# Performance work log

Measured on AMD Instinct MI355X. Metric: run time of the kernel, lower is better.

The kernel has to match this reference:

```python
import jax, jax.numpy as jnp
import numpy as np

E = 128      # embedding_dim
H = 128      # hidden_dim
A = 4        # n_ary
DEPTH = 8    # complete 4-ary tree depth (root at level 0)
N_NODES = (A ** (DEPTH + 1) - 1) // (A - 1)  # 87381


def setup_inputs() -> dict:
    key = jax.random.key(0)
    ks = jax.random.split(key, 11)
    s = 0.05  # weight scale to keep gates in a sane range
    return {
        "embeddings": jax.random.normal(ks[0], (N_NODES, E), jnp.float32),
        "W_iou": jax.random.normal(ks[1], (3 * H, E), jnp.float32) * s,
        "b_iou": jax.random.normal(ks[2], (3 * H,), jnp.float32) * s,
        "U_iou": jax.random.normal(ks[3], (3 * H, A * H), jnp.float32) * s,
        "b_uiou": jax.random.normal(ks[4], (3 * H,), jnp.float32) * s,
        "W_f": jax.random.normal(ks[5], (H, E), jnp.float32) * s,
        "b_wf": jax.random.normal(ks[6], (H,), jnp.float32) * s,
        "U_f": jax.random.normal(ks[7], (A * H, A * H), jnp.float32) * s,
        "b_uf": jax.random.normal(ks[8], (A * H,), jnp.float32) * s,
        "h0": jax.random.uniform(ks[9], (1, A * H), jnp.float32),
        "c0": jax.random.uniform(ks[10], (1, A * H), jnp.float32),
    }


def _tree_lstm_cell(x, h, c, W_iou, b_iou, U_iou, b_uiou, W_f, b_wf, U_f, b_uf):
    # x: [n, E], h/c: [n, A*H]
    n = x.shape[0]
    iou = x @ W_iou.T + b_iou + h @ U_iou.T + b_uiou          # [n, 3H]
    i, o, u = jnp.split(iou, 3, axis=1)
    # forget gates: one per child slot, broadcast W_f(x) over arity dim
    f = jax.nn.sigmoid((h @ U_f.T + b_uf).reshape(n, A, H)
                       + (x @ W_f.T + b_wf)[:, None, :])       # [n, A, H]
    c_new = jax.nn.sigmoid(i) * jnp.tanh(u) + jnp.sum(f * c.reshape(n, A, H), axis=1)
    h_new = jax.nn.sigmoid(o) * jnp.tanh(c_new)
    return h_new, c_new


def reference(embeddings, W_iou, b_iou, U_iou, b_uiou, W_f, b_wf, U_f, b_uf, h0, c0):
    # Level-synchronized bottom-up pass over a complete 4-ary tree of depth DEPTH.
    # embeddings are ordered deepest-level-first; children of parent i at level l
    # are nodes 4i..4i+3 of level l+1.
    hs, cs = [], []
    off = 0
    n_leaf = A ** DEPTH
    h_in = jnp.tile(h0, (n_leaf, 1))  # leaves use learned initial state
    c_in = jnp.tile(c0, (n_leaf, 1))
    for l in range(DEPTH, -1, -1):
        n = A ** l
        x = embeddings[off:off + n]
        h_new, c_new = _tree_lstm_cell(x, h_in, c_in,
                                       W_iou, b_iou, U_iou, b_uiou,
                                       W_f, b_wf, U_f, b_uf)
        hs.append(h_new)
        cs.append(c_new)
        off += n
        if l > 0:
            # pack each parent's A children states into one [A*H] vector
            h_in = h_new.reshape(n // A, A * H)
            c_in = c_new.reshape(n // A, A * H)
    out_h = jnp.concatenate(hs, axis=0)[None]  # [1, N_NODES, H]
    out_c = jnp.concatenate(cs, axis=0)[None]  # [1, N_NODES, H]
    return out_h, out_c
```

## Files before the change

### kernel.cpp

```cpp
#include <hip/hip_runtime.h>
#include <hip/hip_bf16.h>

#define NNODES   87381
#define KIN      640
#define NOUTS    896
#define WC_ELEMS (NOUTS * KIN)
#define DG_STRIDE  71680
#define KT_STRIDE2 3584

typedef __attribute__((ext_vector_type(8))) unsigned short ushort8;
typedef __attribute__((ext_vector_type(4))) unsigned short ushort4v;
typedef __attribute__((ext_vector_type(8))) __bf16        bf16x8;
typedef __attribute__((ext_vector_type(4))) float         f32x4;

union Frag8 { ushort8 u; bf16x8 b; };

__device__ __forceinline__ unsigned short f2bf(float f) {
    unsigned int x = __float_as_uint(f);
    x += 0x7fffu + ((x >> 16) & 1u);
    return (unsigned short)(x >> 16);
}
__device__ __forceinline__ float sigf(float x) {
    return __builtin_amdgcn_rcpf(1.0f + __expf(-x));
}
__device__ __forceinline__ float tanh_fast(float x) { return 2.0f * sigf(2.0f * x) - 1.0f; }

__global__ __launch_bounds__(512) void build_wc(
    const float* __restrict__ W_iou, const float* __restrict__ U_iou,
    const float* __restrict__ W_f,   const float* __restrict__ U_f,
    unsigned short* __restrict__ Wc)
{
    int idx = blockIdx.x * 512 + threadIdx.x;
    if (idx >= WC_ELEMS) return;
    int dg = idx / DG_STRIDE;
    int r  = idx - dg * DG_STRIDE;
    int kt = r / KT_STRIDE2;
    int r2 = r - kt * KT_STRIDE2;
    int cf = r2 >> 9;
    int r3 = r2 & 511;
    int ln = r3 >> 3;
    int j  = r3 & 7;
    int out = cf * 128 + dg * 16 + (ln & 15);
    int k   = kt * 32 + ((ln >> 4) << 3) + j;
    float v;
    if (out < 384) {
        v = (k < 128) ? W_iou[out * 128 + k] : U_iou[(size_t)out * 512 + (k - 128)];
    } else {
        int o2 = out - 384;
        v = (k < 128) ? W_f[(o2 & 127) * 128 + k] : U_f[(size_t)o2 * 512 + (k - 128)];
    }
    Wc[idx] = f2bf(v);
}

__global__ __launch_bounds__(512) void build_consts(
    const float* __restrict__ U_iou, const float* __restrict__ U_f,
    const float* __restrict__ b_iou, const float* __restrict__ b_uiou,
    const float* __restrict__ b_wf,  const float* __restrict__ b_uf,
    const float* __restrict__ h0,
    float* __restrict__ biasc, float* __restrict__ hUc)
{
    const int o  = blockIdx.x * 8 + (threadIdx.x >> 6);
    const int ln = threadIdx.x & 63;
    if (o >= NOUTS) return;
    const float* Urow = (o < 384) ? (U_iou + (size_t)o * 512)
                                  : (U_f + (size_t)(o - 384) * 512);
    const float4 u0 = *(const float4*)(Urow + ln * 8);
    const float4 u1 = *(const float4*)(Urow + ln * 8 + 4);
    const float4 h0v = *(const float4*)(h0 + ln * 8);
    const float4 h1v = *(const float4*)(h0 + ln * 8 + 4);
    float s = u0.x*h0v.x + u0.y*h0v.y + u0.z*h0v.z + u0.w*h0v.w
            + u1.x*h1v.x + u1.y*h1v.y + u1.z*h1v.z + u1.w*h1v.w;
    #pragma unroll
    for (int w = 32; w >= 1; w >>= 1) s += __shfl_xor(s, w);
    if (ln == 0) {
        float b = (o < 384) ? (b_iou[o] + b_uiou[o])
                            : (b_wf[(o - 384) & 127] + b_uf[o - 384]);
        biasc[o] = b;
        hUc[o]   = b + s;
    }
}

__global__ __launch_bounds__(512) void tree_leaf32(
    const float* __restrict__ emb, const unsigned short* __restrict__ Wc,
    const float* __restrict__ hUc, const float* __restrict__ c0,
    float* __restrict__ outh, float* __restrict__ outc,
    unsigned short* __restrict__ hb)
{
    __shared__ __align__(16) char lds[8192];
    const int tid   = threadIdx.x;
    const int node0 = blockIdx.x * 32;

    {
        const int srow = tid >> 4;
        const int sc4  = (tid & 15) << 2;
        const float* src = emb + (size_t)(node0 + srow) * 128;
        const float4 v0 = *(const float4*)(src + sc4);
        const float4 v1 = *(const float4*)(src + 64 + sc4);
        const unsigned wby = (unsigned)((srow * 128 + sc4 * 2) ^ ((srow & 7) << 4));
        ushort4v w0, w1;
        w0[0] = f2bf(v0.x); w0[1] = f2bf(v0.y); w0[2] = f2bf(v0.z); w0[3] = f2bf(v0.w);
        w1[0] = f2bf(v1.x); w1[1] = f2bf(v1.y); w1[2] = f2bf(v1.z); w1[3] = f2bf(v1.w);
        *(ushort4v*)(lds + wby)        = w0;
        *(ushort4v*)(lds + 4096 + wby) = w1;
    }
    __syncthreads();

    const int wv = tid >> 6, ln = tid & 63, grp = ln >> 4, cl = ln & 15;
    const unsigned short* wbase = Wc + (size_t)wv * DG_STRIDE + (size_t)ln * 8;

    f32x4 acc[2][7] = {};
    #pragma unroll
    for (int kt = 0; kt < 4; ++kt) {
        const unsigned short* kp = wbase + kt * KT_STRIDE2;
        Frag8 bfr[7];
        #pragma unroll
        for (int cf = 0; cf < 7; ++cf)
            bfr[cf].u = *(const ushort8*)(kp + cf * 512);
        #pragma unroll
        for (int rf = 0; rf < 2; ++rf) {
            const int row = rf * 16 + cl;
            Frag8 afr;
            afr.u = *(const ushort8*)(lds + (kt >> 1) * 4096 + row * 128
                                      + (((kt & 1) * 64 + grp * 16) ^ ((row & 7) << 4)));
            #pragma unroll
            for (int cf = 0; cf < 7; ++cf)
                acc[rf][cf] = __builtin_amdgcn_mfma_f32_16x16x32_bf16(
                    afr.b, bfr[cf].b, acc[rf][cf], 0, 0, 0);
        }
    }

    const int d = wv * 16 + cl;
    const float bi = hUc[d];
    const float bo = hUc[128 + d];
    const float bu = hUc[256 + d];
    float bfa[4], cin_leaf[4];
    #pragma unroll
    for (int a = 0; a < 4; ++a) { bfa[a] = hUc[384 + a * 128 + d]; cin_leaf[a] = c0[a * 128 + d]; }

    #pragma unroll
    for (int rf = 0; rf < 2; ++rf) {
        #pragma unroll
        for (int reg = 0; reg < 4; ++reg) {
            const int m = node0 + rf * 16 + grp * 4 + reg;
            const float i_ = acc[rf][0][reg] + bi;
            const float o_ = acc[rf][1][reg] + bo;
            const float u_ = acc[rf][2][reg] + bu;
            float c_ = sigf(i_) * tanh_fast(u_);
            #pragma unroll
            for (int a = 0; a < 4; ++a)
                c_ += sigf(acc[rf][3 + a][reg] + bfa[a]) * cin_leaf[a];
            const float h_ = sigf(o_) * tanh_fast(c_);
            const size_t oidx = (size_t)m * 128 + d;
            outh[oidx] = h_;
            outc[oidx] = c_;
            hb[oidx]   = f2bf(h_);
        }
    }
}

__global__ __launch_bounds__(512) void tree_dsplit(
    const float* __restrict__ emb, const unsigned short* __restrict__ Wc,
    const float* __restrict__ biasc,
    float* __restrict__ outh, float* __restrict__ outc,
    unsigned short* __restrict__ hb,
    int n, int off, int cb)
{
    __shared__ __align__(16) char lds[43008];
    const int tid   = threadIdx.x;
    const int mt    = blockIdx.x >> 3;
    const int dg    = blockIdx.x & 7;
    const int node0 = mt * 32;

    {
        const int srow = tid >> 4;
        const int sc4  = (tid & 15) << 2;
        int r = node0 + srow; if (r >= n) r = n - 1;
        const unsigned wby = (unsigned)((srow * 128 + sc4 * 2) ^ ((srow & 7) << 4));
        const float4 v0 = *(const float4*)(emb + (size_t)(off + r) * 128 + sc4);
        const float4 v1 = *(const float4*)(emb + (size_t)(off + r) * 128 + 64 + sc4);
        ushort4v w[10];
        #pragma unroll
        for (int i = 2; i < 10; ++i)
            w[i] = *(const ushort4v*)(hb + (size_t)(cb + 4 * r + ((i - 2) >> 1)) * 128
                                         + ((i - 2) & 1) * 64 + sc4);
        w[0][0] = f2bf(v0.x); w[0][1] = f2bf(v0.y); w[0][2] = f2bf(v0.z); w[0][3] = f2bf(v0.w);
        w[1][0] = f2bf(v1.x); w[1][1] = f2bf(v1.y); w[1][2] = f2bf(v1.z); w[1][3] = f2bf(v1.w);
        #pragma unroll
        for (int i = 0; i < 10; ++i)
            *(ushort4v*)(lds + i * 4096 + wby) = w[i];
    }
    __syncthreads();

    const int wv  = tid >> 6;
    const int ln  = tid & 63;
    const int grp = ln >> 4;
    const int cl  = ln & 15;
    const int rf  = wv & 1;
    const int kq  = wv >> 1;
    const int row = rf * 16 + cl;
    const int swr = (row & 7) << 4;

    const unsigned short* wbase = Wc + (size_t)dg * DG_STRIDE + (size_t)ln * 8
                                     + (size_t)(kq * 5) * KT_STRIDE2;

    f32x4 acc[7] = {};
    #pragma unroll
    for (int t = 0; t < 5; ++t) {
        const int kt = kq * 5 + t;
        Frag8 afr;
        afr.u = *(const ushort8*)(lds + (kt >> 1) * 4096 + row * 128
                                  + (((kt & 1) * 64 + grp * 16) ^ swr));
        const unsigned short* kp = wbase + t * KT_STRIDE2;
        Frag8 bfr[7];
        #pragma unroll
        for (int cf = 0; cf < 7; ++cf)
            bfr[cf].u = *(const ushort8*)(kp + cf * 512);
        #pragma unroll
        for (int cf = 0; cf < 7; ++cf)
            acc[cf] = __builtin_amdgcn_mfma_f32_16x16x32_bf16(
                afr.b, bfr[cf].b, acc[cf], 0, 0, 0);
    }
    __syncthreads();

    float* red = (float*)lds;
    if (kq != 0) {
        const int slot = (((kq - 1) * 2 + rf) * 64 + ln) * 28;
        #pragma unroll
        for (int cf = 0; cf < 7; ++cf)
            *(f32x4*)(red + slot + cf * 4) = acc[cf];
    }
    __syncthreads();
    if (kq == 0) {
        #pragma unroll
        for (int q = 1; q < 4; ++q) {
            const int s2 = (((q - 1) * 2 + rf) * 64 + ln) * 28;
            #pragma unroll
            for (int cf = 0; cf < 7; ++cf)
                acc[cf] += *(const f32x4*)(red + s2 + cf * 4);
        }
        const int d = dg * 16 + cl;
        const float bi = biasc[d];
        const float bo = biasc[128 + d];
        const float bu = biasc[256 + d];
        float bfa[4];
        #pragma unroll
        for (int a = 0; a < 4; ++a) bfa[a] = biasc[384 + a * 128 + d];

        #pragma unroll
        for (int reg = 0; reg < 4; ++reg) {
            const int m = node0 + rf * 16 + grp * 4 + reg;
            if (m < n) {
                const float i_ = acc[0][reg] + bi;
                const float o_ = acc[1][reg] + bo;
                const float u_ = acc[2][reg] + bu;
                float c_ = sigf(i_) * tanh_fast(u_);
                #pragma unroll
                for (int a = 0; a < 4; ++a)
                    c_ += sigf(acc[3 + a][reg] + bfa[a]) * outc[(size_t)(cb + 4 * m + a) * 128 + d];
                const float h_ = sigf(o_) * tanh_fast(c_);
                const size_t oidx = (size_t)(off + m) * 128 + d;
                outh[oidx] = h_;
                outc[oidx] = c_;
                hb[oidx]   = f2bf(h_);
            }
        }
    }
}

__global__ __launch_bounds__(512) void tree_tail3(
    const float* __restrict__ emb, const unsigned short* __restrict__ Wc,
    const float* __restrict__ biasc,
    float* __restrict__ outh, float* __restrict__ outc,
    unsigned short* __restrict__ hb)
{
    __shared__ __align__(16) char lds[40960];
    const int ns[3]   = {16, 4, 1};
    const int offs[3] = {87360, 87376, 87380};
    const int cbs[3]  = {87296, 87360, 87376};

    const int tid = threadIdx.x;
    const int wv = tid >> 6, ln = tid & 63, grp = ln >> 4, cl = ln & 15;

    #pragma unroll 1
    for (int li = 0; li < 3; ++li) {
        const int n = ns[li], off = offs[li], cb = cbs[li];

        if (tid < 256) {
            const int srow = tid >> 4;
            const int sc4  = (tid & 15) << 2;
            int r = srow; if (r >= n) r = n - 1;
            const unsigned wby = (unsigned)((srow * 128 + sc4 * 2) ^ ((srow & 7) << 4));
            const float4 v0 = *(const float4*)(emb + (size_t)(off + r) * 128 + sc4);
            const float4 v1 = *(const float4*)(emb + (size_t)(off + r) * 128 + 64 + sc4);
            ushort4v w0, w1;
            w0[0] = f2bf(v0.x); w0[1] = f2bf(v0.y); w0[2] = f2bf(v0.z); w0[3] = f2bf(v0.w);
            w1[0] = f2bf(v1.x); w1[1] = f2bf(v1.y); w1[2] = f2bf(v1.z); w1[3] = f2bf(v1.w);
            *(ushort4v*)(lds + wby)        = w0;
            *(ushort4v*)(lds + 4096 + wby) = w1;
            #pragma unroll
            for (int i = 2; i < 10; ++i) {
                ushort4v w = *(const ushort4v*)(hb + (size_t)(cb + 4 * r + ((i - 2) >> 1)) * 128
                                                   + ((i - 2) & 1) * 64 + sc4);
                *(ushort4v*)(lds + i * 4096 + wby) = w;
            }
        }
        __syncthreads();

        const unsigned short* wbase = Wc + (size_t)wv * DG_STRIDE + (size_t)ln * 8;
        f32x4 acc[7] = {};
        #pragma unroll 2
        for (int kt = 0; kt < 20; ++kt) {
            Frag8 afr;
            afr.u = *(const ushort8*)(lds + (kt >> 1) * 4096 + cl * 128
                                      + (((kt & 1) * 64 + grp * 16) ^ ((cl & 7) << 4)));
            const unsigned short* kp = wbase + kt * KT_STRIDE2;
            Frag8 bfr[7];
            #pragma unroll
            for (int cf = 0; cf < 7; ++cf)
                bfr[cf].u = *(const ushort8*)(kp + cf * 512);
            #pragma unroll
            for (int cf = 0; cf < 7; ++cf)
                acc[cf] = __builtin_amdgcn_mfma_f32_16x16x32_bf16(
                    afr.b, bfr[cf].b, acc[cf], 0, 0, 0);
        }

        const int d = wv * 16 + cl;
        const float bi = biasc[d];
        const float bo = biasc[128 + d];
        const float bu = biasc[256 + d];
        float bfa[4];
        #pragma unroll
        for (int a = 0; a < 4; ++a) bfa[a] = biasc[384 + a * 128 + d];

        #pragma unroll
        for (int reg = 0; reg < 4; ++reg) {
            const int m = grp * 4 + reg;
            if (m < n) {
                const float i_ = acc[0][reg] + bi;
                const float o_ = acc[1][reg] + bo;
                const float u_ = acc[2][reg] + bu;
                float c_ = sigf(i_) * tanh_fast(u_);
                #pragma unroll
                for (int a = 0; a < 4; ++a)
                    c_ += sigf(acc[3 + a][reg] + bfa[a]) * outc[(size_t)(cb + 4 * m + a) * 128 + d];
                const float h_ = sigf(o_) * tanh_fast(c_);
                const size_t oidx = (size_t)(off + m) * 128 + d;
                outh[oidx] = h_;
                outc[oidx] = c_;
                hb[oidx]   = f2bf(h_);
            }
        }
        __threadfence();
        __syncthreads();
    }
}

extern "C" void kernel_launch(void* const* d_in, const int* in_sizes, int n_in,
                              void* d_out, int out_size, void* d_ws, size_t ws_size,
                              hipStream_t stream)
{
    const float* emb    = (const float*)d_in[0];
    const float* W_iou  = (const float*)d_in[1];
    const float* b_iou  = (const float*)d_in[2];
    const float* U_iou  = (const float*)d_in[3];
    const float* b_uiou = (const float*)d_in[4];
    const float* W_f    = (const float*)d_in[5];
    const float* b_wf   = (const float*)d_in[6];
    const float* U_f    = (const float*)d_in[7];
    const float* b_uf   = (const float*)d_in[8];
    const float* h0     = (const float*)d_in[9];
    const float* c0     = (const float*)d_in[10];

    char* ws = (char*)d_ws;
    unsigned short* Wc  = (unsigned short*)ws;
    float* biasc        = (float*)(ws + 1146880);
    float* hUc          = (float*)(ws + 1150464);
    unsigned short* hb  = (unsigned short*)(ws + 1154112);

    float* outh = (float*)d_out;
    float* outc = outh + (size_t)NNODES * 128;

    hipLaunchKernelGGL(build_wc, dim3((WC_ELEMS + 511) / 512), dim3(512), 0, stream,
                       W_iou, U_iou, W_f, U_f, Wc);
    hipLaunchKernelGGL(build_consts, dim3(NOUTS / 8), dim3(512), 0, stream,
                       U_iou, U_f, b_iou, b_uiou, b_wf, b_uf, h0, biasc, hUc);

    hipLaunchKernelGGL(tree_leaf32, dim3(2048), dim3(512), 0, stream,
                       emb, Wc, hUc, c0, outh, outc, hb);

    const int ns[5]   = {16384, 4096, 1024, 256, 64};
    const int offs[5] = {65536, 81920, 86016, 87040, 87296};
    const int cbs[5]  = {0, 65536, 81920, 86016, 87040};
    for (int li = 0; li < 5; ++li) {
        const int units = (ns[li] / 32) * 8;
        hipLaunchKernelGGL(tree_dsplit, dim3(units), dim3(512), 0, stream,
                           emb, Wc, biasc, outh, outc, hb,
                           ns[li], offs[li], cbs[li]);
    }

    hipLaunchKernelGGL(tree_tail3, dim3(1), dim3(512), 0, stream,
                       emb, Wc, biasc, outh, outc, hb);
}
```

Before: 320.8 us.

## Merge prep kernels, widen staging loads, remap blocks per XCD, double-buffer weight fragments

Fuses the weight-packing and bias/constant kernels into a single prep launch to save one launch. Staging loads of embeddings and child hidden states now use 16-byte vectors, so each thread issues fewer global and LDS operations. tree_dsplit remaps block indices so that consecutive node tiles land on the same XCD, which should improve L2 locality. It also double-buffers the weight B-fragments across k-steps to overlap global loads with MFMA, at the cost of more registers.

```diff
diff --git a/kernel.cpp b/kernel.cpp
--- a/kernel.cpp
+++ b/kernel.cpp
@@ -9,7 +9,6 @@
 #define KT_STRIDE2 3584
 
 typedef __attribute__((ext_vector_type(8))) unsigned short ushort8;
-typedef __attribute__((ext_vector_type(4))) unsigned short ushort4v;
 typedef __attribute__((ext_vector_type(8))) __bf16        bf16x8;
 typedef __attribute__((ext_vector_type(4))) float         f32x4;
 
@@ -25,58 +24,61 @@
 }
 __device__ __forceinline__ float tanh_fast(float x) { return 2.0f * sigf(2.0f * x) - 1.0f; }
 
-__global__ __launch_bounds__(512) void build_wc(
+__device__ __forceinline__ ushort8 pack8(const float4& v0, const float4& v1) {
+    ushort8 w;
+    w[0] = f2bf(v0.x); w[1] = f2bf(v0.y); w[2] = f2bf(v0.z); w[3] = f2bf(v0.w);
+    w[4] = f2bf(v1.x); w[5] = f2bf(v1.y); w[6] = f2bf(v1.z); w[7] = f2bf(v1.w);
+    return w;
+}
+
+__global__ __launch_bounds__(512) void prep(
     const float* __restrict__ W_iou, const float* __restrict__ U_iou,
     const float* __restrict__ W_f,   const float* __restrict__ U_f,
-    unsigned short* __restrict__ Wc)
-{
-    int idx = blockIdx.x * 512 + threadIdx.x;
-    if (idx >= WC_ELEMS) return;
-    int dg = idx / DG_STRIDE;
-    int r  = idx - dg * DG_STRIDE;
-    int kt = r / KT_STRIDE2;
-    int r2 = r - kt * KT_STRIDE2;
-    int cf = r2 >> 9;
-    int r3 = r2 & 511;
-    int ln = r3 >> 3;
-    int j  = r3 & 7;
-    int out = cf * 128 + dg * 16 + (ln & 15);
-    int k   = kt * 32 + ((ln >> 4) << 3) + j;
-    float v;
-    if (out < 384) {
-        v = (k < 128) ? W_iou[out * 128 + k] : U_iou[(size_t)out * 512 + (k - 128)];
-    } else {
-        int o2 = out - 384;
-        v = (k < 128) ? W_f[(o2 & 127) * 128 + k] : U_f[(size_t)o2 * 512 + (k - 128)];
-    }
-    Wc[idx] = f2bf(v);
-}
-
-__global__ __launch_bounds__(512) void build_consts(
-    const float* __restrict__ U_iou, const float* __restrict__ U_f,
     const float* __restrict__ b_iou, const float* __restrict__ b_uiou,
     const float* __restrict__ b_wf,  const float* __restrict__ b_uf,
     const float* __restrict__ h0,
-    float* __restrict__ biasc, float* __restrict__ hUc)
+    unsigned short* __restrict__ Wc, float* __restrict__ biasc, float* __restrict__ hUc)
 {
-    const int o  = blockIdx.x * 8 + (threadIdx.x >> 6);
-    const int ln = threadIdx.x & 63;
-    if (o >= NOUTS) return;
-    const float* Urow = (o < 384) ? (U_iou + (size_t)o * 512)
-                                  : (U_f + (size_t)(o - 384) * 512);
-    const float4 u0 = *(const float4*)(Urow + ln * 8);
-    const float4 u1 = *(const float4*)(Urow + ln * 8 + 4);
-    const float4 h0v = *(const float4*)(h0 + ln * 8);
-    const float4 h1v = *(const float4*)(h0 + ln * 8 + 4);
-    float s = u0.x*h0v.x + u0.y*h0v.y + u0.z*h0v.z + u0.w*h0v.w
-            + u1.x*h1v.x + u1.y*h1v.y + u1.z*h1v.z + u1.w*h1v.w;
-    #pragma unroll
-    for (int w = 32; w >= 1; w >>= 1) s += __shfl_xor(s, w);
-    if (ln == 0) {
-        float b = (o < 384) ? (b_iou[o] + b_uiou[o])
-                            : (b_wf[(o - 384) & 127] + b_uf[o - 384]);
-        biasc[o] = b;
-        hUc[o]   = b + s;
+    if (blockIdx.x < 1120) {
+        int idx = blockIdx.x * 512 + threadIdx.x;
+        int dg = idx / DG_STRIDE;
+        int r  = idx - dg * DG_STRIDE;
+        int kt = r / KT_STRIDE2;
+        int r2 = r - kt * KT_STRIDE2;
+        int cf = r2 >> 9;
+        int r3 = r2 & 511;
+        int ln = r3 >> 3;
+        int j  = r3 & 7;
+        int out = cf * 128 + dg * 16 + (ln & 15);
+        int k   = kt * 32 + ((ln >> 4) << 3) + j;
+        float v;
+        if (out < 384) {
+            v = (k < 128) ? W_iou[out * 128 + k] : U_iou[(size_t)out * 512 + (k - 128)];
+        } else {
+            int o2 = out - 384;
+            v = (k < 128) ? W_f[(o2 & 127) * 128 + k] : U_f[(size_t)o2 * 512 + (k - 128)];
+        }
+        Wc[idx] = f2bf(v);
+    } else {
+        const int o  = (blockIdx.x - 1120) * 8 + (threadIdx.x >> 6);
+        const int ln = threadIdx.x & 63;
+        if (o >= NOUTS) return;
+        const float* Urow = (o < 384) ? (U_iou + (size_t)o * 512)
+                                      : (U_f + (size_t)(o - 384) * 512);
+        const float4 u0 = *(const float4*)(Urow + ln * 8);
+        const float4 u1 = *(const float4*)(Urow + ln * 8 + 4);
+        const float4 h0v = *(const float4*)(h0 + ln * 8);
+        const float4 h1v = *(const float4*)(h0 + ln * 8 + 4);
+        float s = u0.x*h0v.x + u0.y*h0v.y + u0.z*h0v.z + u0.w*h0v.w
+                + u1.x*h1v.x + u1.y*h1v.y + u1.z*h1v.z + u1.w*h1v.w;
+        #pragma unroll
+        for (int w = 32; w >= 1; w >>= 1) s += __shfl_xor(s, w);
+        if (ln == 0) {
+            float b = (o < 384) ? (b_iou[o] + b_uiou[o])
+                                : (b_wf[(o - 384) & 127] + b_uf[o - 384]);
+            biasc[o] = b;
+            hUc[o]   = b + s;
+        }
     }
 }
 
@@ -92,16 +94,13 @@
 
     {
         const int srow = tid >> 4;
-        const int sc4  = (tid & 15) << 2;
-        const float* src = emb + (size_t)(node0 + srow) * 128;
-        const float4 v0 = *(const float4*)(src + sc4);
-        const float4 v1 = *(const float4*)(src + 64 + sc4);
-        const unsigned wby = (unsigned)((srow * 128 + sc4 * 2) ^ ((srow & 7) << 4));
-        ushort4v w0, w1;
-        w0[0] = f2bf(v0.x); w0[1] = f2bf(v0.y); w0[2] = f2bf(v0.z); w0[3] = f2bf(v0.w);
-        w1[0] = f2bf(v1.x); w1[1] = f2bf(v1.y); w1[2] = f2bf(v1.z); w1[3] = f2bf(v1.w);
-        *(ushort4v*)(lds + wby)        = w0;
-        *(ushort4v*)(lds + 4096 + wby) = w1;
+        const int q    = tid & 15;
+        const float* src = emb + (size_t)(node0 + srow) * 128 + q * 8;
+        const float4 v0 = *(const float4*)src;
+        const float4 v1 = *(const float4*)(src + 4);
+        const int stripe = q >> 3;
+        const unsigned by = (unsigned)((srow * 128 + (q & 7) * 16) ^ ((srow & 7) << 4));
+        *(ushort8*)(lds + stripe * 4096 + by) = pack8(v0, v1);
     }
     __syncthreads();
 
@@ -166,28 +165,44 @@
     int n, int off, int cb)
 {
     __shared__ __align__(16) char lds[43008];
-    const int tid   = threadIdx.x;
-    const int mt    = blockIdx.x >> 3;
-    const int dg    = blockIdx.x & 7;
+    const int tid = threadIdx.x;
+    const int nmt = n >> 5;
+
+    int mt, dg;
+    if (nmt >= 8) {
+        const int xcd = blockIdx.x & 7;
+        const int j   = blockIdx.x >> 3;
+        mt = xcd * (nmt >> 3) + (j >> 3);
+        dg = j & 7;
+    } else {
+        mt = blockIdx.x >> 3;
+        dg = blockIdx.x & 7;
+    }
     const int node0 = mt * 32;
 
     {
         const int srow = tid >> 4;
-        const int sc4  = (tid & 15) << 2;
+        const int q    = tid & 15;
         int r = node0 + srow; if (r >= n) r = n - 1;
-        const unsigned wby = (unsigned)((srow * 128 + sc4 * 2) ^ ((srow & 7) << 4));
-        const float4 v0 = *(const float4*)(emb + (size_t)(off + r) * 128 + sc4);
-        const float4 v1 = *(const float4*)(emb + (size_t)(off + r) * 128 + 64 + sc4);
-        ushort4v w[10];
-        #pragma unroll
-        for (int i = 2; i < 10; ++i)
-            w[i] = *(const ushort4v*)(hb + (size_t)(cb + 4 * r + ((i - 2) >> 1)) * 128
-                                         + ((i - 2) & 1) * 64 + sc4);
-        w[0][0] = f2bf(v0.x); w[0][1] = f2bf(v0.y); w[0][2] = f2bf(v0.z); w[0][3] = f2bf(v0.w);
-        w[1][0] = f2bf(v1.x); w[1][1] = f2bf(v1.y); w[1][2] = f2bf(v1.z); w[1][3] = f2bf(v1.w);
-        #pragma unroll
-        for (int i = 0; i < 10; ++i)
-            *(ushort4v*)(lds + i * 4096 + wby) = w[i];
+        const unsigned sx = (unsigned)((srow & 7) << 4);
+        {
+            const float* s = emb + (size_t)(off + r) * 128 + q * 8;
+            const float4 v0 = *(const float4*)s;
+            const float4 v1 = *(const float4*)(s + 4);
+            const int stripe = q >> 3;
+            const unsigned by = (unsigned)((srow * 128 + (q & 7) * 16) ^ sx);
+            *(ushort8*)(lds + stripe * 4096 + by) = pack8(v0, v1);
+        }
+        #pragma unroll
+        for (int c = 1; c < 5; ++c) {
+            const int e = c * 128 + q * 8;
+            const int child = (e - 128) >> 7;
+            const int d0    = (e - 128) & 127;
+            ushort8 w = *(const ushort8*)(hb + (size_t)(cb + 4 * r + child) * 128 + d0);
+            const int stripe = e >> 6;
+            const unsigned by = (unsigned)((srow * 128 + (e & 63) * 2) ^ sx);
+            *(ushort8*)(lds + stripe * 4096 + by) = w;
+        }
     }
     __syncthreads();
 
@@ -203,22 +218,29 @@
     const unsigned short* wbase = Wc + (size_t)dg * DG_STRIDE + (size_t)ln * 8
                                      + (size_t)(kq * 5) * KT_STRIDE2;
 
+    Frag8 bb[2][7];
+    #pragma unroll
+    for (int cf = 0; cf < 7; ++cf)
+        bb[0][cf].u = *(const ushort8*)(wbase + cf * 512);
+
     f32x4 acc[7] = {};
     #pragma unroll
     for (int t = 0; t < 5; ++t) {
+        const int cur = t & 1, nxt = cur ^ 1;
+        if (t < 4) {
+            const unsigned short* kp = wbase + (t + 1) * KT_STRIDE2;
+            #pragma unroll
+            for (int cf = 0; cf < 7; ++cf)
+                bb[nxt][cf].u = *(const ushort8*)(kp + cf * 512);
+        }
         const int kt = kq * 5 + t;
         Frag8 afr;
         afr.u = *(const ushort8*)(lds + (kt >> 1) * 4096 + row * 128
                                   + (((kt & 1) * 64 + grp * 16) ^ swr));
-        const unsigned short* kp = wbase + t * KT_STRIDE2;
-        Frag8 bfr[7];
-        #pragma unroll
-        for (int cf = 0; cf < 7; ++cf)
-            bfr[cf].u = *(const ushort8*)(kp + cf * 512);
         #pragma unroll
         for (int cf = 0; cf < 7; ++cf)
             acc[cf] = __builtin_amdgcn_mfma_f32_16x16x32_bf16(
-                afr.b, bfr[cf].b, acc[cf], 0, 0, 0);
+                afr.b, bb[cur][cf].b, acc[cf], 0, 0, 0);
     }
     __syncthreads();
 
@@ -287,21 +309,24 @@
 
         if (tid < 256) {
             const int srow = tid >> 4;
-            const int sc4  = (tid & 15) << 2;
+            const int q    = tid & 15;
             int r = srow; if (r >= n) r = n - 1;
-            const unsigned wby = (unsigned)((srow * 128 + sc4 * 2) ^ ((srow & 7) << 4));
-            const float4 v0 = *(const float4*)(emb + (size_t)(off + r) * 128 + sc4);
-            const float4 v1 = *(const float4*)(emb + (size_t)(off + r) * 128 + 64 + sc4);
-            ushort4v w0, w1;
-            w0[0] = f2bf(v0.x); w0[1] = f2bf(v0.y); w0[2] = f2bf(v0.z); w0[3] = f2bf(v0.w);
-            w1[0] = f2bf(v1.x); w1[1] = f2bf(v1.y); w1[2] = f2bf(v1.z); w1[3] = f2bf(v1.w);
-            *(ushort4v*)(lds + wby)        = w0;
-            *(ushort4v*)(lds + 4096 + wby) = w1;
-            #pragma unroll
-            for (int i = 2; i < 10; ++i) {
-                ushort4v w = *(const ushort4v*)(hb + (size_t)(cb + 4 * r + ((i - 2) >> 1)) * 128
-                                                   + ((i - 2) & 1) * 64 + sc4);
-                *(ushort4v*)(lds + i * 4096 + wby) = w;
+            const unsigned sx = (unsigned)((srow & 7) << 4);
+            {
+                const float* s = emb + (size_t)(off + r) * 128 + q * 8;
+                const float4 v0 = *(const float4*)s;
+                const float4 v1 = *(const float4*)(s + 4);
+                const unsigned by = (unsigned)((srow * 128 + (q & 7) * 16) ^ sx);
+                *(ushort8*)(lds + (q >> 3) * 4096 + by) = pack8(v0, v1);
+            }
+            #pragma unroll
+            for (int c = 1; c < 5; ++c) {
+                const int e = c * 128 + q * 8;
+                const int child = (e - 128) >> 7;
+                const int d0    = (e - 128) & 127;
+                ushort8 w = *(const ushort8*)(hb + (size_t)(cb + 4 * r + child) * 128 + d0);
+                const unsigned by = (unsigned)((srow * 128 + (e & 63) * 2) ^ sx);
+                *(ushort8*)(lds + (e >> 6) * 4096 + by) = w;
             }
         }
         __syncthreads();
@@ -380,10 +405,9 @@
     float* outh = (float*)d_out;
     float* outc = outh + (size_t)NNODES * 128;
 
-    hipLaunchKernelGGL(build_wc, dim3((WC_ELEMS + 511) / 512), dim3(512), 0, stream,
-                       W_iou, U_iou, W_f, U_f, Wc);
-    hipLaunchKernelGGL(build_consts, dim3(NOUTS / 8), dim3(512), 0, stream,
-                       U_iou, U_f, b_iou, b_uiou, b_wf, b_uf, h0, biasc, hUc);
+    hipLaunchKernelGGL(prep, dim3(1232), dim3(512), 0, stream,
+                       W_iou, U_iou, W_f, U_f, b_iou, b_uiou, b_wf, b_uf, h0,
+                       Wc, biasc, hUc);
 
     hipLaunchKernelGGL(tree_leaf32, dim3(2048), dim3(512), 0, stream,
                        emb, Wc, hUc, c0, outh, outc, hb);
```

After: 294.4 us. 1.09x faster.
